# Performance work log

Measured on AMD Instinct MI355X. Metric: run time of the kernel, lower is better.

## Reference

```python
import jax, jax.numpy as jnp
import numpy as np

N, E, D, HGC, LG, NC = 20000, 320000, 256, 256, 4, 2
BN_EPS = 1e-5


def setup_inputs() -> dict:
    key = jax.random.key(0)
    ks = jax.random.split(key, 12)
    features = jax.random.normal(ks[0], (N, D), jnp.float32)
    edge_index = jax.random.randint(ks[1], (2, E), 0, N)
    edgenet_input = jax.random.uniform(ks[2], (E, 6), dtype=jnp.float32)
    edge_weight_override = jax.random.uniform(ks[3], (E,), dtype=jnp.float32)
    # ChebConv weights: K=3 weight matrices per layer; layer0 in=D==HGC so one stack works
    cheb_w = jax.random.normal(ks[4], (LG, 3, HGC, HGC), jnp.float32) * np.float32((2.0 / HGC) ** 0.5)
    w1 = jax.random.normal(ks[5], (LG * HGC, 256), jnp.float32) * np.float32((2.0 / (LG * HGC)) ** 0.5)
    b1 = jnp.zeros((256,), jnp.float32)
    bn_gamma = jnp.ones((256,), jnp.float32)
    bn_beta = jnp.zeros((256,), jnp.float32)
    bn_mean = jnp.zeros((256,), jnp.float32)
    bn_var = jnp.ones((256,), jnp.float32)
    w2 = jax.random.normal(ks[6], (256, NC), jnp.float32) * np.float32((2.0 / 256.0) ** 0.5)
    b2 = jnp.zeros((NC,), jnp.float32)
    return dict(features=features, edge_index=edge_index, edgenet_input=edgenet_input,
                edge_weight_override=edge_weight_override, cheb_w=cheb_w,
                w1=w1, b1=b1, bn_gamma=bn_gamma, bn_beta=bn_beta,
                bn_mean=bn_mean, bn_var=bn_var, w2=w2, b2=b2)


def reference(features, edge_index, edgenet_input, edge_weight_override, cheb_w,
              w1, b1, bn_gamma, bn_beta, bn_mean, bn_var, w2, b2):
    # eval mode: dropout / edge_dropout are no-ops; edge_weight_override bypasses PAE
    ew = edge_weight_override  # [E]
    row, col = edge_index[0], edge_index[1]  # source, target (PyG source_to_target)
    n = features.shape[0]
    # sym-normalized scaled Laplacian, lambda_max=2: L_hat = -D^{-1/2} A D^{-1/2} (diag 1-1=0)
    deg = jax.ops.segment_sum(ew, row, num_segments=n)
    dis = jnp.where(deg > 0, jax.lax.rsqrt(deg), 0.0)
    norm = -(dis[row] * ew * dis[col])  # [E]

    def prop(x):  # out[col] += norm * x[row]
        return jax.ops.segment_sum(norm[:, None] * x[row], col, num_segments=n)

    def cheb(x, W):  # W: [3, in, out]; Chebyshev recursion T0=x, T1=L_hat x, T2=2 L_hat T1 - T0
        tx0 = x
        tx1 = prop(x)
        out = tx0 @ W[0] + tx1 @ W[1]
        tx2 = 2.0 * prop(tx1) - tx0
        return out + tx2 @ W[2]

    h = jax.nn.relu(cheb(features, cheb_w[0]))
    jk = h
    for i in range(1, cheb_w.shape[0]):
        h = jax.nn.relu(cheb(h, cheb_w[i]))
        jk = jnp.concatenate((jk, h), axis=1)
    # classifier: Linear -> ReLU -> BatchNorm1d(eval) -> Linear
    z = jax.nn.relu(jk @ w1 + b1)
    z = (z - bn_mean) * (bn_gamma * jax.lax.rsqrt(bn_var + BN_EPS)) + bn_beta
    logit = z @ w2 + b2
    return logit, ew
```

## Files before the change

kernel.cpp:

```cpp
#include <hip/hip_runtime.h>
#include <hip/hip_bf16.h>

#define NN 20000
#define EE 320000
#define LGN 4

typedef unsigned short u16;
typedef short bf16x8 __attribute__((ext_vector_type(8)));
typedef float f32x4 __attribute__((ext_vector_type(4)));

__device__ __forceinline__ float bf2f(u16 v) {
    unsigned int u = ((unsigned int)v) << 16;
    float f; __builtin_memcpy(&f, &u, 4); return f;
}
__device__ __forceinline__ u16 f2bf(float f) {
    __hip_bfloat16 h = __float2bfloat16(f);
    u16 u; __builtin_memcpy(&u, &h, 2); return u;
}

__device__ __forceinline__ void gll16(const void* g, void* l) {
    __builtin_amdgcn_global_load_lds(
        (const __attribute__((address_space(1))) unsigned int*)g,
        (__attribute__((address_space(3))) unsigned int*)l, 16, 0, 0);
}

__global__ __launch_bounds__(256) void k_edge1(const int* __restrict__ ei,
                                               const float* __restrict__ ew,
                                               float* __restrict__ deg,
                                               int* __restrict__ counts,
                                               float* __restrict__ out_ew) {
    int e = blockIdx.x * 256 + threadIdx.x;
    if (e >= EE) return;
    int r = ei[e];
    float w = ew[e];
    atomicAdd(&deg[r], w);
    atomicAdd(&counts[ei[EE + e]], 1);
    out_ew[e] = w;
}

__global__ __launch_bounds__(256) void k_rsqrt(float* __restrict__ deg) {
    int i = blockIdx.x * 256 + threadIdx.x;
    if (i >= NN) return;
    float d = deg[i];
    deg[i] = (d > 0.f) ? rsqrtf(d) : 0.f;
}

__global__ __launch_bounds__(1024) void k_scan(const int* __restrict__ counts,
                                               int* __restrict__ offs) {
    __shared__ int part[1024];
    int t = threadIdx.x;
    const int C = (NN + 1023) / 1024;
    int lo = t * C, hi = min(lo + C, NN);
    int s = 0;
    for (int i = lo; i < hi; i++) s += counts[i];
    part[t] = s;
    __syncthreads();
    for (int off = 1; off < 1024; off <<= 1) {
        int add = (t >= off) ? part[t - off] : 0;
        __syncthreads();
        part[t] += add;
        __syncthreads();
    }
    int base = part[t] - s;
    for (int i = lo; i < hi; i++) { offs[i] = base; base += counts[i]; }
    if (t == 1023) offs[NN] = part[1023];
}

__global__ __launch_bounds__(256) void k_scatter(const int* __restrict__ ei,
                                                 const float* __restrict__ ew,
                                                 const float* __restrict__ dis,
                                                 const int* __restrict__ offs,
                                                 int* __restrict__ cursor,
                                                 int2* __restrict__ nbrs) {
    int e = blockIdx.x * 256 + threadIdx.x;
    if (e >= EE) return;
    int r = ei[e], c = ei[EE + e];
    float nm = -(dis[r] * ew[e] * dis[c]);
    int pidx = offs[c] + atomicAdd(&cursor[c], 1);
    nbrs[pidx] = make_int2(r, __float_as_int(nm));
}

__global__ __launch_bounds__(256) void k_cast(const float* __restrict__ src,
                                              u16* __restrict__ dst, int n) {
    int i = blockIdx.x * 256 + threadIdx.x;
    if (i < n) dst[i] = f2bf(src[i]);
}

__global__ __launch_bounds__(256) void k_cast_T(const float* __restrict__ src,
                                                u16* __restrict__ dst, int K) {
    __shared__ u16 tile[32][33];
    int kt = blockIdx.x * 32, nt = blockIdx.y * 32;
    int tx = threadIdx.x & 31, ty = threadIdx.x >> 5;
#pragma unroll
    for (int i = 0; i < 32; i += 8)
        tile[ty + i][tx] = f2bf(src[(size_t)(kt + ty + i) * 256 + (nt + tx)]);
    __syncthreads();
#pragma unroll
    for (int i = 0; i < 32; i += 8)
        dst[(size_t)(nt + ty + i) * K + (kt + tx)] = tile[tx][ty + i];
}

__global__ __launch_bounds__(256) void k_foldbn(const float* __restrict__ g,
                                                const float* __restrict__ be,
                                                const float* __restrict__ mn,
                                                const float* __restrict__ vr,
                                                float* __restrict__ sc,
                                                float* __restrict__ sh) {
    int t = threadIdx.x;
    if (t < 256) {
        float s = g[t] * rsqrtf(vr[t] + 1e-5f);
        sc[t] = s;
        sh[t] = be[t] - mn[t] * s;
    }
}

__global__ __launch_bounds__(256) void k_prop(const u16* __restrict__ x, int ldx,
                                              const u16* __restrict__ xsub, int ldsub,
                                              int dotx2,
                                              u16* __restrict__ out, int ldo,
                                              const int* __restrict__ offs,
                                              const int2* __restrict__ nbrs) {
    int c = __builtin_amdgcn_readfirstlane(blockIdx.x * 4 + (threadIdx.x >> 6));
    int lane = threadIdx.x & 63;
    int s = offs[c], e = offs[c + 1];
    float a0 = 0.f, a1 = 0.f, a2 = 0.f, a3 = 0.f;
    for (int i = s; i < e; i += 8) {
        int2 mm[8];
        ushort4 xv[8];
#pragma unroll
        for (int j = 0; j < 8; j++) mm[j] = nbrs[i + j];
#pragma unroll
        for (int j = 0; j < 8; j++)
            xv[j] = *(const ushort4*)(x + (size_t)mm[j].x * ldx + lane * 4);
#pragma unroll
        for (int j = 0; j < 8; j++) {
            float w = (i + j < e) ? __int_as_float(mm[j].y) : 0.f;
            a0 += w * bf2f(xv[j].x);
            a1 += w * bf2f(xv[j].y);
            a2 += w * bf2f(xv[j].z);
            a3 += w * bf2f(xv[j].w);
        }
    }
    if (dotx2) {
        ushort4 xs = *(const ushort4*)(xsub + (size_t)c * ldsub + lane * 4);
        a0 = 2.f * a0 - bf2f(xs.x);
        a1 = 2.f * a1 - bf2f(xs.y);
        a2 = 2.f * a2 - bf2f(xs.z);
        a3 = 2.f * a3 - bf2f(xs.w);
    }
    ushort4 o;
    o.x = f2bf(a0); o.y = f2bf(a1); o.z = f2bf(a2); o.w = f2bf(a3);
    *(ushort4*)(out + (size_t)c * ldo + lane * 4) = o;
}

__global__ __launch_bounds__(256, 2) void k_gemm(
    const u16* __restrict__ A0, const u16* __restrict__ A1,
    const u16* __restrict__ A2, const u16* __restrict__ A3,
    int lda0, int lda1, int lda2, int lda3,
    int K, const u16* __restrict__ Bt,
    int mode,
    u16* __restrict__ outb, int ldob,
    const float* __restrict__ bias, const float* __restrict__ sc,
    const float* __restrict__ sh,
    const float* __restrict__ w2, const float* __restrict__ b2,
    float* __restrict__ outlog) {
    __shared__ __align__(16) u16 lds[2 * 20 * 512];
    int t = threadIdx.x;
    int wv = t >> 6, l = t & 63;
    int q = l >> 4, l16 = l & 15;
    int m0 = blockIdx.x * 64;
    int n0 = wv * 64;
    const int steps = K >> 5;

    f32x4 acc[4][4] = {};

    int arow = min(m0 + wv * 16 + l16, NN - 1);

    auto stage = [&](int buf, int s) {
        int kt = s * 32;
        u16* base = lds + buf * 20 * 512;
#pragma unroll
        for (int j = 0; j < 4; j++) {
            const u16* bg = Bt + (size_t)((wv * 4 + j) * 16 + l16) * K + kt + q * 8;
            gll16(bg, base + (wv * 4 + j) * 512);
        }
        int ch = kt >> 8;
        const u16* ap;
        int la;
        if (ch == 0) { ap = A0; la = lda0; }
        else if (ch == 1) { ap = A1; la = lda1; }
        else if (ch == 2) { ap = A2; la = lda2; }
        else { ap = A3; la = lda3; }
        gll16(ap + (size_t)arow * la + (kt & 255) + q * 8, base + (16 + wv) * 512);
    };

    stage(0, 0);
    for (int s = 0; s < steps; s++) {
        __syncthreads();
        if (s + 1 < steps) stage((s + 1) & 1, s + 1);
        const u16* base = lds + (s & 1) * 20 * 512;
        bf16x8 a[4], b[4];
#pragma unroll
        for (int mh = 0; mh < 4; mh++)
            a[mh] = *(const bf16x8*)(base + (16 + mh) * 512 + l * 8);
#pragma unroll
        for (int j = 0; j < 4; j++)
            b[j] = *(const bf16x8*)(base + (wv * 4 + j) * 512 + l * 8);
#pragma unroll
        for (int mh = 0; mh < 4; mh++)
#pragma unroll
            for (int j = 0; j < 4; j++)
                acc[mh][j] =
                    __builtin_amdgcn_mfma_f32_16x16x32_bf16(a[mh], b[j], acc[mh][j], 0, 0, 0);
    }
    __syncthreads();

    if (mode == 0) {
        u16* Cs = lds + wv * 4608;
#pragma unroll
        for (int mh = 0; mh < 4; mh++)
#pragma unroll
            for (int j = 0; j < 4; j++)
#pragma unroll
                for (int i = 0; i < 4; i++) {
                    float v = acc[mh][j][i];
                    v = v > 0.f ? v : 0.f;
                    Cs[(mh * 16 + q * 4 + i) * 72 + j * 16 + l16] = f2bf(v);
                }
#pragma unroll
        for (int j = 0; j < 8; j++) {
            int f = j * 64 + l;
            int r = f >> 3, cc = (f & 7) * 8;
            uint4 cv = *(const uint4*)&Cs[r * 72 + cc];
            int row = m0 + r;
            if (row < NN) *(uint4*)(outb + (size_t)row * ldob + n0 + cc) = cv;
        }
    } else {
        float bi[4], s4[4], h4[4], wa[4], wb[4];
#pragma unroll
        for (int j = 0; j < 4; j++) {
            int col = n0 + j * 16 + l16;
            bi[j] = bias[col];
            s4[j] = sc[col];
            h4[j] = sh[col];
            wa[j] = w2[2 * col];
            wb[j] = w2[2 * col + 1];
        }
        float* red = (float*)lds;
#pragma unroll
        for (int mh = 0; mh < 4; mh++)
#pragma unroll
            for (int i = 0; i < 4; i++) {
                float p0 = 0.f, p1 = 0.f;
#pragma unroll
                for (int j = 0; j < 4; j++) {
                    float v = acc[mh][j][i] + bi[j];
                    v = v > 0.f ? v : 0.f;
                    v = v * s4[j] + h4[j];
                    p0 += v * wa[j];
                    p1 += v * wb[j];
                }
#pragma unroll
                for (int off = 1; off < 16; off <<= 1) {
                    p0 += __shfl_xor(p0, off, 64);
                    p1 += __shfl_xor(p1, off, 64);
                }
                if (l16 == 0) {
                    int rl = mh * 16 + q * 4 + i;
                    red[(wv * 64 + rl) * 2 + 0] = p0;
                    red[(wv * 64 + rl) * 2 + 1] = p1;
                }
            }
        __syncthreads();
        if (t < 128) {
            int rl = t >> 1, cp = t & 1;
            float v = red[(0 * 64 + rl) * 2 + cp] + red[(1 * 64 + rl) * 2 + cp] +
                      red[(2 * 64 + rl) * 2 + cp] + red[(3 * 64 + rl) * 2 + cp];
            int row = m0 + rl;
            if (row < NN) outlog[(size_t)row * 2 + cp] = v + b2[cp];
        }
    }
}

extern "C" void kernel_launch(void* const* d_in, const int* in_sizes, int n_in,
                              void* d_out, int out_size, void* d_ws, size_t ws_size,
                              hipStream_t stream) {
    const float* features = (const float*)d_in[0];
    const int* ei = (const int*)d_in[1];
    const float* ew = (const float*)d_in[3];
    const float* cheb_w = (const float*)d_in[4];
    const float* w1 = (const float*)d_in[5];
    const float* b1 = (const float*)d_in[6];
    const float* g = (const float*)d_in[7];
    const float* be = (const float*)d_in[8];
    const float* mn = (const float*)d_in[9];
    const float* vr = (const float*)d_in[10];
    const float* w2 = (const float*)d_in[11];
    const float* b2 = (const float*)d_in[12];
    float* out = (float*)d_out;

    char* p = (char*)d_ws;
    auto alloc = [&](size_t bytes) -> char* {
        char* r = p;
        p += (bytes + 255) & ~(size_t)255;
        return r;
    };
    float* deg = (float*)alloc((size_t)NN * 4);
    int* counts = (int*)alloc((size_t)(NN + 1) * 4);
    int* cursor = (int*)alloc((size_t)NN * 4);
    size_t zero_bytes = (size_t)(p - (char*)deg);
    int* offs = (int*)alloc((size_t)(NN + 1) * 4);
    int2* nbrs = (int2*)alloc((size_t)(EE + 8) * 8);
    u16* xb = (u16*)alloc((size_t)NN * 256 * 2);
    u16* tx1 = (u16*)alloc((size_t)NN * 256 * 2);
    u16* tx2 = (u16*)alloc((size_t)NN * 256 * 2);
    u16* jk = (u16*)alloc((size_t)NN * 1024 * 2);
    u16* chebT = (u16*)alloc((size_t)LGN * 3 * 256 * 256 * 2);
    u16* w1T = (u16*)alloc((size_t)1024 * 256 * 2);
    float* sc = (float*)alloc(256 * 4);
    float* sh = (float*)alloc(256 * 4);

    hipMemsetAsync(deg, 0, zero_bytes, stream);
    hipMemsetAsync(nbrs + EE, 0, 8 * sizeof(int2), stream);
    k_edge1<<<(EE + 255) / 256, 256, 0, stream>>>(ei, ew, deg, counts, out + (size_t)NN * 2);
    k_rsqrt<<<(NN + 255) / 256, 256, 0, stream>>>(deg);
    k_scan<<<1, 1024, 0, stream>>>(counts, offs);
    k_scatter<<<(EE + 255) / 256, 256, 0, stream>>>(ei, ew, deg, offs, cursor, nbrs);
    k_cast<<<((NN * 256) + 255) / 256, 256, 0, stream>>>(features, xb, NN * 256);
    for (int i = 0; i < LGN; i++)
        k_cast_T<<<dim3(24, 8), 256, 0, stream>>>(cheb_w + (size_t)i * 768 * 256,
                                                  chebT + (size_t)i * 256 * 768, 768);
    k_cast_T<<<dim3(32, 8), 256, 0, stream>>>(w1, w1T, 1024);
    k_foldbn<<<1, 256, 0, stream>>>(g, be, mn, vr, sc, sh);

    const int gg = (NN + 63) / 64;
    for (int i = 0; i < LGN; i++) {
        const u16* x = (i == 0) ? xb : (jk + (size_t)(i - 1) * 256);
        int ldx = (i == 0) ? 256 : 1024;
        k_prop<<<NN / 4, 256, 0, stream>>>(x, ldx, (const u16*)nullptr, 0, 0, tx1, 256, offs,
                                           nbrs);
        k_prop<<<NN / 4, 256, 0, stream>>>(tx1, 256, x, ldx, 1, tx2, 256, offs, nbrs);
        k_gemm<<<gg, 256, 0, stream>>>(
            x, tx1, tx2, (const u16*)nullptr, ldx, 256, 256, 0, 768,
            chebT + (size_t)i * 256 * 768, 0, jk + (size_t)i * 256, 1024, (const float*)nullptr,
            (const float*)nullptr, (const float*)nullptr, (const float*)nullptr,
            (const float*)nullptr, (float*)nullptr);
    }
    k_gemm<<<gg, 256, 0, stream>>>(jk, jk + 256, jk + 512, jk + 768, 1024, 1024, 1024, 1024,
                                   1024, w1T, 1, (u16*)nullptr, 0, b1, sc, sh, w2, b2, out);
}
```

Baseline: 526.9 us.

## Load GEMM B fragments from pre-swizzled global layout and deepen A-stage pipeline

Weights are now cast into a fragment-major layout so each wave can load its B operands straight into registers, skipping LDS. LDS then holds only A tiles in a 4-deep ring, driven by explicit vmcnt waits and raw barriers, and occupancy is raised to 3 blocks per SM. The sparse propagation kernel now processes 16 neighbours per iteration, with a conditional second batch, to keep more gathers in flight. The risks are more register pressure, and hand-coded vmcnt counts that must exactly match the number of issued loads.

```diff
diff --git a/kernel.cpp b/kernel.cpp
--- a/kernel.cpp
+++ b/kernel.cpp
@@ -86,18 +86,17 @@
     if (i < n) dst[i] = f2bf(src[i]);
 }
 
-__global__ __launch_bounds__(256) void k_cast_T(const float* __restrict__ src,
-                                                u16* __restrict__ dst, int K) {
-    __shared__ u16 tile[32][33];
-    int kt = blockIdx.x * 32, nt = blockIdx.y * 32;
-    int tx = threadIdx.x & 31, ty = threadIdx.x >> 5;
-#pragma unroll
-    for (int i = 0; i < 32; i += 8)
-        tile[ty + i][tx] = f2bf(src[(size_t)(kt + ty + i) * 256 + (nt + tx)]);
-    __syncthreads();
-#pragma unroll
-    for (int i = 0; i < 32; i += 8)
-        dst[(size_t)(nt + ty + i) * K + (kt + tx)] = tile[tx][ty + i];
+__global__ __launch_bounds__(256) void k_castB(const float* __restrict__ src,
+                                               u16* __restrict__ dst, int K) {
+    int tid = blockIdx.x * 256 + threadIdx.x;
+    if (tid >= (K >> 5) * 1024) return;
+    int l = tid & 63, f = (tid >> 6) & 15, s = tid >> 10;
+    int col = f * 16 + (l & 15);
+    int kb = s * 32 + ((l >> 4) << 3);
+    u16 tmp[8];
+#pragma unroll
+    for (int j = 0; j < 8; j++) tmp[j] = f2bf(src[(size_t)(kb + j) * 256 + col]);
+    *(uint4*)(dst + (size_t)tid * 8) = *(uint4*)tmp;
 }
 
 __global__ __launch_bounds__(256) void k_foldbn(const float* __restrict__ g,
@@ -124,14 +123,22 @@
     int lane = threadIdx.x & 63;
     int s = offs[c], e = offs[c + 1];
     float a0 = 0.f, a1 = 0.f, a2 = 0.f, a3 = 0.f;
-    for (int i = s; i < e; i += 8) {
-        int2 mm[8];
-        ushort4 xv[8];
+    for (int i = s; i < e; i += 16) {
+        int2 mm[16];
+        ushort4 xv[16];
 #pragma unroll
         for (int j = 0; j < 8; j++) mm[j] = nbrs[i + j];
 #pragma unroll
         for (int j = 0; j < 8; j++)
             xv[j] = *(const ushort4*)(x + (size_t)mm[j].x * ldx + lane * 4);
+        bool more = (i + 8 < e);
+        if (more) {
+#pragma unroll
+            for (int j = 8; j < 16; j++) mm[j] = nbrs[i + j];
+#pragma unroll
+            for (int j = 8; j < 16; j++)
+                xv[j] = *(const ushort4*)(x + (size_t)mm[j].x * ldx + lane * 4);
+        }
 #pragma unroll
         for (int j = 0; j < 8; j++) {
             float w = (i + j < e) ? __int_as_float(mm[j].y) : 0.f;
@@ -140,6 +147,16 @@
             a2 += w * bf2f(xv[j].z);
             a3 += w * bf2f(xv[j].w);
         }
+        if (more) {
+#pragma unroll
+            for (int j = 8; j < 16; j++) {
+                float w = (i + j < e) ? __int_as_float(mm[j].y) : 0.f;
+                a0 += w * bf2f(xv[j].x);
+                a1 += w * bf2f(xv[j].y);
+                a2 += w * bf2f(xv[j].z);
+                a3 += w * bf2f(xv[j].w);
+            }
+        }
     }
     if (dotx2) {
         ushort4 xs = *(const ushort4*)(xsub + (size_t)c * ldsub + lane * 4);
@@ -153,18 +170,18 @@
     *(ushort4*)(out + (size_t)c * ldo + lane * 4) = o;
 }
 
-__global__ __launch_bounds__(256, 2) void k_gemm(
+__global__ __launch_bounds__(256, 3) void k_gemm(
     const u16* __restrict__ A0, const u16* __restrict__ A1,
     const u16* __restrict__ A2, const u16* __restrict__ A3,
     int lda0, int lda1, int lda2, int lda3,
-    int K, const u16* __restrict__ Bt,
+    int K, const u16* __restrict__ Bf,
     int mode,
     u16* __restrict__ outb, int ldob,
     const float* __restrict__ bias, const float* __restrict__ sc,
     const float* __restrict__ sh,
     const float* __restrict__ w2, const float* __restrict__ b2,
     float* __restrict__ outlog) {
-    __shared__ __align__(16) u16 lds[2 * 20 * 512];
+    __shared__ __align__(16) u16 lds[18432];
     int t = threadIdx.x;
     int wv = t >> 6, l = t & 63;
     int q = l >> 4, l16 = l & 15;
@@ -176,14 +193,8 @@
 
     int arow = min(m0 + wv * 16 + l16, NN - 1);
 
-    auto stage = [&](int buf, int s) {
+    auto stageA = [&](int buf, int s) {
         int kt = s * 32;
-        u16* base = lds + buf * 20 * 512;
-#pragma unroll
-        for (int j = 0; j < 4; j++) {
-            const u16* bg = Bt + (size_t)((wv * 4 + j) * 16 + l16) * K + kt + q * 8;
-            gll16(bg, base + (wv * 4 + j) * 512);
-        }
         int ch = kt >> 8;
         const u16* ap;
         int la;
@@ -191,27 +202,55 @@
         else if (ch == 1) { ap = A1; la = lda1; }
         else if (ch == 2) { ap = A2; la = lda2; }
         else { ap = A3; la = lda3; }
-        gll16(ap + (size_t)arow * la + (kt & 255) + q * 8, base + (16 + wv) * 512);
+        gll16(ap + (size_t)arow * la + (kt & 255) + q * 8, lds + buf * 2048 + wv * 512);
     };
 
-    stage(0, 0);
-    for (int s = 0; s < steps; s++) {
-        __syncthreads();
-        if (s + 1 < steps) stage((s + 1) & 1, s + 1);
-        const u16* base = lds + (s & 1) * 20 * 512;
-        bf16x8 a[4], b[4];
+    const u16* bfw = Bf + (size_t)(wv * 4) * 512 + l * 8;
+    auto loadB = [&](bf16x8* dst, int s) {
+#pragma unroll
+        for (int j = 0; j < 4; j++)
+            dst[j] = *(const bf16x8*)(bfw + (size_t)s * 8192 + j * 512);
+    };
+    auto comp = [&](int buf, const bf16x8* b) {
+        const u16* base = lds + buf * 2048;
+        bf16x8 a[4];
 #pragma unroll
         for (int mh = 0; mh < 4; mh++)
-            a[mh] = *(const bf16x8*)(base + (16 + mh) * 512 + l * 8);
-#pragma unroll
-        for (int j = 0; j < 4; j++)
-            b[j] = *(const bf16x8*)(base + (wv * 4 + j) * 512 + l * 8);
+            a[mh] = *(const bf16x8*)(base + mh * 512 + l * 8);
 #pragma unroll
         for (int mh = 0; mh < 4; mh++)
 #pragma unroll
             for (int j = 0; j < 4; j++)
                 acc[mh][j] =
                     __builtin_amdgcn_mfma_f32_16x16x32_bf16(a[mh], b[j], acc[mh][j], 0, 0, 0);
+    };
+
+    bf16x8 bA[4], bB[4];
+    loadB(bA, 0);
+    stageA(0, 0);
+    stageA(1, 1);
+    stageA(2, 2);
+    for (int s = 0; s < steps; s += 2) {
+        if (s == 0)               asm volatile("s_waitcnt vmcnt(2)" ::: "memory");
+        else if (s == steps - 2)  asm volatile("s_waitcnt vmcnt(9)" ::: "memory");
+        else                      asm volatile("s_waitcnt vmcnt(10)" ::: "memory");
+        __builtin_amdgcn_s_barrier();
+        __builtin_amdgcn_sched_barrier(0);
+        loadB(bB, s + 1);
+        __builtin_amdgcn_sched_barrier(0);
+        if (s + 3 < steps) stageA((s + 3) & 3, s + 3);
+        __builtin_amdgcn_sched_barrier(0);
+        comp(s & 3, bA);
+        if (s == 0)               asm volatile("s_waitcnt vmcnt(6)" ::: "memory");
+        else if (s == steps - 2)  asm volatile("s_waitcnt vmcnt(8)" ::: "memory");
+        else                      asm volatile("s_waitcnt vmcnt(10)" ::: "memory");
+        __builtin_amdgcn_s_barrier();
+        __builtin_amdgcn_sched_barrier(0);
+        if (s + 2 < steps) loadB(bA, s + 2);
+        __builtin_amdgcn_sched_barrier(0);
+        if (s + 4 < steps) stageA((s + 4) & 3, s + 4);
+        __builtin_amdgcn_sched_barrier(0);
+        comp((s + 1) & 3, bB);
     }
     __syncthreads();
 
@@ -310,7 +349,7 @@
     int* cursor = (int*)alloc((size_t)NN * 4);
     size_t zero_bytes = (size_t)(p - (char*)deg);
     int* offs = (int*)alloc((size_t)(NN + 1) * 4);
-    int2* nbrs = (int2*)alloc((size_t)(EE + 8) * 8);
+    int2* nbrs = (int2*)alloc((size_t)(EE + 16) * 8);
     u16* xb = (u16*)alloc((size_t)NN * 256 * 2);
     u16* tx1 = (u16*)alloc((size_t)NN * 256 * 2);
     u16* tx2 = (u16*)alloc((size_t)NN * 256 * 2);
@@ -321,16 +360,16 @@
     float* sh = (float*)alloc(256 * 4);
 
     hipMemsetAsync(deg, 0, zero_bytes, stream);
-    hipMemsetAsync(nbrs + EE, 0, 8 * sizeof(int2), stream);
+    hipMemsetAsync(nbrs + EE, 0, 16 * sizeof(int2), stream);
     k_edge1<<<(EE + 255) / 256, 256, 0, stream>>>(ei, ew, deg, counts, out + (size_t)NN * 2);
     k_rsqrt<<<(NN + 255) / 256, 256, 0, stream>>>(deg);
     k_scan<<<1, 1024, 0, stream>>>(counts, offs);
     k_scatter<<<(EE + 255) / 256, 256, 0, stream>>>(ei, ew, deg, offs, cursor, nbrs);
     k_cast<<<((NN * 256) + 255) / 256, 256, 0, stream>>>(features, xb, NN * 256);
     for (int i = 0; i < LGN; i++)
-        k_cast_T<<<dim3(24, 8), 256, 0, stream>>>(cheb_w + (size_t)i * 768 * 256,
-                                                  chebT + (size_t)i * 256 * 768, 768);
-    k_cast_T<<<dim3(32, 8), 256, 0, stream>>>(w1, w1T, 1024);
+        k_castB<<<96, 256, 0, stream>>>(cheb_w + (size_t)i * 768 * 256,
+                                        chebT + (size_t)i * 256 * 768, 768);
+    k_castB<<<128, 256, 0, stream>>>(w1, w1T, 1024);
     k_foldbn<<<1, 256, 0, stream>>>(g, be, mn, vr, sc, sh);
 
     const int gg = (NN + 63) / 64;
```

Result: faster. 458.7 us (-12.9%).
